# Kernel tuning notes

Hardware: AMD Instinct MI355X
Metric: run time of the kernel (lower is better)

The kernel has to match this reference:

```python
import jax, jax.numpy as jnp
import numpy as np

B, S, D = 2, 4096, 4096          # batch, seq, hidden == qkv_output_dim
R = 16                            # LoRA rank
BOTTLE = 64                       # policy bottleneck
SCALING = 2.0                     # all_scalings for both adapters
CAT = 2 * D                       # input_multiplier = 1 + num_active_adapters(=1)


def setup_inputs() -> dict:
    key = jax.random.key(0)
    ks = jax.random.split(key, 16)
    s = 0.02
    return {
        "x": jax.random.normal(ks[0], (B, S, D), jnp.float32),
        "base_out": jax.random.normal(ks[1], (B, S, D), jnp.float32),
        # LoRA banks: A [r, hidden], B [out, r]
        "A_pos": jax.random.normal(ks[2], (R, D), jnp.float32) * s,
        "B_pos": jax.random.normal(ks[3], (D, R), jnp.float32) * s,
        "A_neg": jax.random.normal(ks[4], (R, D), jnp.float32) * s,
        "B_neg": jax.random.normal(ks[5], (D, R), jnp.float32) * s,
        # policy direction net: Linear(CAT->64) -> ReLU -> Linear(64->D)
        "W1": jax.random.normal(ks[6], (BOTTLE, CAT), jnp.float32) * s,
        "b1": jnp.zeros((BOTTLE,), jnp.float32),
        "W2": jax.random.normal(ks[7], (D, BOTTLE), jnp.float32) * s,
        "b2": jnp.zeros((D,), jnp.float32),
        # policy gate net: Linear(CAT->64) -> ReLU -> Linear(64->1)
        "G1": jax.random.normal(ks[8], (BOTTLE, CAT), jnp.float32) * s,
        "g1": jnp.zeros((BOTTLE,), jnp.float32),
        "G2": jax.random.normal(ks[9], (1, BOTTLE), jnp.float32) * 0.01,
        "g2": jnp.zeros((1,), jnp.float32),
    }


def reference(x, base_out, A_pos, B_pos, A_neg, B_neg,
              W1, b1, W2, b2, G1, g1, G2, g2):
    # hook_fn: sum of two LoRA deltas (low-rank: contract to rank first)
    lora = ((x @ A_pos.T) @ B_pos.T) * SCALING + ((x @ A_neg.T) @ B_neg.T) * SCALING  # [B,S,D]
    # FusionPolicy with a single (summed) adapter input
    cat_input = jnp.concatenate([base_out, lora], axis=-1)  # [B,S,2D]
    residual_base = lora
    h = jax.nn.relu(cat_input @ W1.T + b1)                  # [B,S,64]
    direction = h @ W2.T + b2 + residual_base               # [B,S,D]
    hg = jax.nn.relu(cat_input @ G1.T + g1)                 # [B,S,64]
    alpha = jax.nn.sigmoid((hg @ G2.T + g2) * 6.0)          # [B,S,1]
    fusion_delta = direction * alpha
    return base_out + fusion_delta
```

## Files before the change

kernel.cpp:

```cpp
#include <hip/hip_runtime.h>
#include <math.h>

#define BSROWS 8192
#define DD 4096
#define CATD 8192
#define NB 64
#define NP1 160
#define PS 164
#define HS 104
#define KOUT 96

typedef __attribute__((ext_vector_type(8))) short bf16x8;
typedef __attribute__((ext_vector_type(4))) float f32x4;

static __device__ __forceinline__ unsigned short f2bf(float f) {
  union { float f; unsigned u; } v; v.f = f;
  unsigned r = v.u + 0x7FFFu + ((v.u >> 16) & 1u);
  return (unsigned short)(r >> 16);
}

static __device__ __forceinline__ bf16x8 pack8(const float* __restrict__ p) {
  float4 a = *(const float4*)p;
  float4 b = *(const float4*)(p + 4);
  bf16x8 r;
  r[0] = (short)f2bf(a.x); r[1] = (short)f2bf(a.y);
  r[2] = (short)f2bf(a.z); r[3] = (short)f2bf(a.w);
  r[4] = (short)f2bf(b.x); r[5] = (short)f2bf(b.y);
  r[6] = (short)f2bf(b.z); r[7] = (short)f2bf(b.w);
  return r;
}

__global__ void prep_weights(const float* __restrict__ A_pos, const float* __restrict__ A_neg,
                             const float* __restrict__ W1, const float* __restrict__ G1,
                             const float* __restrict__ W2, const float* __restrict__ B_pos,
                             const float* __restrict__ B_neg,
                             unsigned short* __restrict__ Wp1, unsigned short* __restrict__ Wout) {
  int tid = blockIdx.x * blockDim.x + threadIdx.x;
  const int total = NP1 * DD + DD * KOUT;
  for (int e = tid; e < total; e += gridDim.x * blockDim.x) {
    if (e < NP1 * DD) {
      int n = e >> 12, k = e & 4095;
      float v;
      if (n < 16)      v = A_pos[n * DD + k];
      else if (n < 32) v = A_neg[(n - 16) * DD + k];
      else if (n < 96) v = W1[(n - 32) * CATD + k];
      else             v = G1[(n - 96) * CATD + k];
      Wp1[e] = f2bf(v);
    } else {
      int e2 = e - NP1 * DD;
      int n = e2 / KOUT, j = e2 - n * KOUT;
      float v;
      if (j < NB) v = W2[n * NB + j];
      else {
        int i = j - NB;
        v = 2.f * ((i < 16) ? B_pos[n * 16 + i] : B_neg[n * 16 + (i - 16)]);
      }
      Wout[e2] = f2bf(v);
    }
  }
}

__global__ void prep_m_partial(const float* __restrict__ B_pos, const float* __restrict__ B_neg,
                               const float* __restrict__ W1, const float* __restrict__ G1,
                               float* __restrict__ part) {
  int t = blockIdx.x * 256 + threadIdx.x;
  int chunk = t >> 12;
  int rem = t & 4095;
  int net = rem >> 11;
  int i = (rem >> 6) & 31;
  int j = rem & 63;
  const float* Bp = (i < 16) ? (B_pos + i) : (B_neg + (i - 16));
  const float* Wr = ((net == 0) ? W1 : G1) + (size_t)j * CATD + DD;
  float acc = 0.f;
  int d0 = chunk * 512;
#pragma unroll 8
  for (int d = 0; d < 512; ++d) acc += Bp[(size_t)(d0 + d) * 16] * Wr[d0 + d];
  part[t] = 2.f * acc;
}

__global__ void prep_m_reduce(const float* __restrict__ part,
                              float* __restrict__ M1, float* __restrict__ M2) {
  int t = blockIdx.x * 256 + threadIdx.x;
  int net = t >> 11;
  int ij = t & 2047;
  float s = 0.f;
#pragma unroll
  for (int c = 0; c < 8; ++c) s += part[c * 4096 + net * 2048 + ij];
  (net == 0 ? M1 : M2)[ij] = s;
}

__global__ __launch_bounds__(512, 4)
void fused_main(const float* __restrict__ x, const float* __restrict__ base,
                const unsigned short* __restrict__ Wp1, const unsigned short* __restrict__ Wout,
                const float* __restrict__ M1, const float* __restrict__ M2,
                const float* __restrict__ b1, const float* __restrict__ g1,
                const float* __restrict__ b2f, const float* __restrict__ G2,
                const float* __restrict__ g2, float* __restrict__ out) {
  __shared__ __align__(16) float P[2][16][PS];
  __shared__ __align__(16) unsigned short Hcat[16][HS];
  __shared__ float alpha_s[16];

  const int tid = threadIdx.x;
  const int w = tid >> 6;
  const int lane = tid & 63;
  const int col = lane & 15;
  const int kseg = (lane >> 4) * 8;
  const int kh = w >> 2;
  const int wsub = w & 3;
  const long row0 = (long)blockIdx.x * 16;

  const float* xrow = x + (row0 + col) * DD;
  const float* brow = base + (row0 + col) * DD;

  f32x4 acc0 = {0.f, 0.f, 0.f, 0.f};
  f32x4 acc1 = {0.f, 0.f, 0.f, 0.f};
  f32x4 acc2 = {0.f, 0.f, 0.f, 0.f};
  const bool hasx = (wsub < 2);
  const int kbeg = kh * 2048;
#pragma unroll 2
  for (int k0 = kbeg; k0 < kbeg + 2048; k0 += 32) {
    const int kk = k0 + kseg;
    bf16x8 ba = pack8(brow + kk);
    bf16x8 a0;
    if (hasx) a0 = pack8(xrow + kk); else a0 = ba;
    const unsigned short* wp = Wp1 + kk;
    bf16x8 bw0 = *(const bf16x8*)(wp + (size_t)(wsub * 16 + col) * DD);
    bf16x8 bw1 = *(const bf16x8*)(wp + (size_t)((wsub + 4) * 16 + col) * DD);
    acc0 = __builtin_amdgcn_mfma_f32_16x16x32_bf16(a0, bw0, acc0, 0, 0, 0);
    acc1 = __builtin_amdgcn_mfma_f32_16x16x32_bf16(ba, bw1, acc1, 0, 0, 0);
    if (hasx) {
      bf16x8 bw2 = *(const bf16x8*)(wp + (size_t)((wsub + 8) * 16 + col) * DD);
      acc2 = __builtin_amdgcn_mfma_f32_16x16x32_bf16(ba, bw2, acc2, 0, 0, 0);
    }
  }
  {
    const int rbase = (lane >> 4) * 4;
#pragma unroll
    for (int r = 0; r < 4; ++r) {
      P[kh][rbase + r][wsub * 16 + col] = acc0[r];
      P[kh][rbase + r][(wsub + 4) * 16 + col] = acc1[r];
      if (hasx) P[kh][rbase + r][(wsub + 8) * 16 + col] = acc2[r];
    }
  }
  __syncthreads();

  if (tid < 256) {
    const int row = tid >> 4, jg = tid & 15;
    float tl[32];
#pragma unroll
    for (int i = 0; i < 32; ++i) tl[i] = P[0][row][i] + P[1][row][i];
    float hv[4];
    float partg = 0.f;
#pragma unroll
    for (int jj = 0; jj < 4; ++jj) {
      const int j = jg * 4 + jj;
      float s1 = b1[j] + P[0][row][32 + j] + P[1][row][32 + j];
      float s2 = g1[j] + P[0][row][96 + j] + P[1][row][96 + j];
#pragma unroll
      for (int i = 0; i < 32; ++i) {
        s1 += tl[i] * M1[i * 64 + j];
        s2 += tl[i] * M2[i * 64 + j];
      }
      hv[jj] = fmaxf(s1, 0.f);
      partg += G2[j] * fmaxf(s2, 0.f);
    }
#pragma unroll
    for (int m = 8; m >= 1; m >>= 1) partg += __shfl_xor(partg, m);
    const float alpha = 1.f / (1.f + expf(-6.f * (partg + g2[0])));
    if (jg == 0) alpha_s[row] = alpha;
#pragma unroll
    for (int jj = 0; jj < 4; ++jj) Hcat[row][jg * 4 + jj] = f2bf(alpha * hv[jj]);
    if (jg < 8) {
#pragma unroll
      for (int ii = 0; ii < 4; ++ii)
        Hcat[row][64 + jg * 4 + ii] = f2bf(alpha * tl[jg * 4 + ii]);
    }
  }
  __syncthreads();

  bf16x8 af0 = *(const bf16x8*)&Hcat[col][kseg];
  bf16x8 af1 = *(const bf16x8*)&Hcat[col][32 + kseg];
  bf16x8 af2 = *(const bf16x8*)&Hcat[col][64 + kseg];
  const int rbase = (lane >> 4) * 4;
  float al[4];
#pragma unroll
  for (int r = 0; r < 4; ++r) al[r] = alpha_s[rbase + r];

  for (int i = 0; i < 32; ++i) {
    const int nt = w + 8 * i;
    const int gcol = nt * 16 + col;
    const unsigned short* wo = Wout + (size_t)gcol * KOUT;
    bf16x8 w0 = *(const bf16x8*)(wo + kseg);
    bf16x8 w1v = *(const bf16x8*)(wo + 32 + kseg);
    bf16x8 w2v = *(const bf16x8*)(wo + 64 + kseg);
    f32x4 c = {0.f, 0.f, 0.f, 0.f};
    c = __builtin_amdgcn_mfma_f32_16x16x32_bf16(af0, w0, c, 0, 0, 0);
    c = __builtin_amdgcn_mfma_f32_16x16x32_bf16(af1, w1v, c, 0, 0, 0);
    c = __builtin_amdgcn_mfma_f32_16x16x32_bf16(af2, w2v, c, 0, 0, 0);
    const float bb = b2f[gcol];
#pragma unroll
    for (int r = 0; r < 4; ++r) {
      const size_t off = (size_t)(row0 + rbase + r) * DD + gcol;
      out[off] = base[off] + c[r] + al[r] * bb;
    }
  }
}

extern "C" void kernel_launch(void* const* d_in, const int* in_sizes, int n_in,
                              void* d_out, int out_size, void* d_ws, size_t ws_size,
                              hipStream_t stream) {
  const float* x     = (const float*)d_in[0];
  const float* base  = (const float*)d_in[1];
  const float* A_pos = (const float*)d_in[2];
  const float* B_pos = (const float*)d_in[3];
  const float* A_neg = (const float*)d_in[4];
  const float* B_neg = (const float*)d_in[5];
  const float* W1    = (const float*)d_in[6];
  const float* b1    = (const float*)d_in[7];
  const float* W2    = (const float*)d_in[8];
  const float* b2    = (const float*)d_in[9];
  const float* G1    = (const float*)d_in[10];
  const float* g1    = (const float*)d_in[11];
  const float* G2    = (const float*)d_in[12];
  const float* g2    = (const float*)d_in[13];
  float* out = (float*)d_out;

  char* ws = (char*)d_ws;
  unsigned short* Wp1  = (unsigned short*)(ws);
  unsigned short* Wout = (unsigned short*)(ws + 1310720);
  float* M1   = (float*)(ws + 2097152);
  float* M2   = (float*)(ws + 2105344);
  float* part = (float*)(ws + 2113536);

  prep_weights<<<1024, 256, 0, stream>>>(A_pos, A_neg, W1, G1, W2, B_pos, B_neg, Wp1, Wout);
  prep_m_partial<<<128, 256, 0, stream>>>(B_pos, B_neg, W1, G1, part);
  prep_m_reduce<<<16, 256, 0, stream>>>(part, M1, M2);
  fused_main<<<512, 512, 0, stream>>>(x, base, Wp1, Wout, M1, M2, b1, g1, b2, G2, g2, out);
}
```

Before: 547.9 us.

## Split fused main kernel into panel, policy and output GEMM stages for more parallelism

The single fused kernel, one block per 16-row tile and 512 blocks total, is split into three kernels. panel_P splits K across two blocks and writes partial projections to global memory. policy_rows computes the gate and hidden activations per row. out_gemm splits the output columns four ways across 2048 blocks. The M-matrix precompute also becomes a single warp-reduction kernel instead of partial plus reduce. The aim is more blocks and occupancy on the many-CU GPU, at the cost of extra global round trips for the partial sums and Hcat, extra launches, and base being read twice.

```diff
diff --git a/kernel.cpp b/kernel.cpp
--- a/kernel.cpp
+++ b/kernel.cpp
@@ -7,7 +7,6 @@
 #define NB 64
 #define NP1 160
 #define PS 164
-#define HS 104
 #define KOUT 96
 
 typedef __attribute__((ext_vector_type(8))) short bf16x8;
@@ -60,45 +59,28 @@
   }
 }
 
-__global__ void prep_m_partial(const float* __restrict__ B_pos, const float* __restrict__ B_neg,
-                               const float* __restrict__ W1, const float* __restrict__ G1,
-                               float* __restrict__ part) {
-  int t = blockIdx.x * 256 + threadIdx.x;
-  int chunk = t >> 12;
-  int rem = t & 4095;
-  int net = rem >> 11;
-  int i = (rem >> 6) & 31;
-  int j = rem & 63;
+__global__ __launch_bounds__(256, 8)
+void prep_m(const float* __restrict__ B_pos, const float* __restrict__ B_neg,
+            const float* __restrict__ W1, const float* __restrict__ G1,
+            float* __restrict__ M1, float* __restrict__ M2) {
+  const int wid = blockIdx.x * 4 + (threadIdx.x >> 6);
+  const int lane = threadIdx.x & 63;
+  const int net = wid >> 11, ij = wid & 2047;
+  const int i = ij >> 6, j = ij & 63;
   const float* Bp = (i < 16) ? (B_pos + i) : (B_neg + (i - 16));
   const float* Wr = ((net == 0) ? W1 : G1) + (size_t)j * CATD + DD;
   float acc = 0.f;
-  int d0 = chunk * 512;
-#pragma unroll 8
-  for (int d = 0; d < 512; ++d) acc += Bp[(size_t)(d0 + d) * 16] * Wr[d0 + d];
-  part[t] = 2.f * acc;
-}
-
-__global__ void prep_m_reduce(const float* __restrict__ part,
-                              float* __restrict__ M1, float* __restrict__ M2) {
-  int t = blockIdx.x * 256 + threadIdx.x;
-  int net = t >> 11;
-  int ij = t & 2047;
-  float s = 0.f;
-#pragma unroll
-  for (int c = 0; c < 8; ++c) s += part[c * 4096 + net * 2048 + ij];
-  (net == 0 ? M1 : M2)[ij] = s;
-}
-
-__global__ __launch_bounds__(512, 4)
-void fused_main(const float* __restrict__ x, const float* __restrict__ base,
-                const unsigned short* __restrict__ Wp1, const unsigned short* __restrict__ Wout,
-                const float* __restrict__ M1, const float* __restrict__ M2,
-                const float* __restrict__ b1, const float* __restrict__ g1,
-                const float* __restrict__ b2f, const float* __restrict__ G2,
-                const float* __restrict__ g2, float* __restrict__ out) {
+  for (int d = lane; d < DD; d += 64)
+    acc += Bp[(size_t)d * 16] * Wr[d];
+#pragma unroll
+  for (int m = 32; m >= 1; m >>= 1) acc += __shfl_xor(acc, m);
+  if (lane == 0) (net == 0 ? M1 : M2)[ij] = 2.f * acc;
+}
+
+__global__ __launch_bounds__(512, 8)
+void panel_P(const float* __restrict__ x, const float* __restrict__ base,
+             const unsigned short* __restrict__ Wp1, float* __restrict__ Ppart) {
   __shared__ __align__(16) float P[2][16][PS];
-  __shared__ __align__(16) unsigned short Hcat[16][HS];
-  __shared__ float alpha_s[16];
 
   const int tid = threadIdx.x;
   const int w = tid >> 6;
@@ -107,7 +89,9 @@
   const int kseg = (lane >> 4) * 8;
   const int kh = w >> 2;
   const int wsub = w & 3;
-  const long row0 = (long)blockIdx.x * 16;
+  const int tile = blockIdx.x >> 1;
+  const int bkh = blockIdx.x & 1;
+  const long row0 = (long)tile * 16;
 
   const float* xrow = x + (row0 + col) * DD;
   const float* brow = base + (row0 + col) * DD;
@@ -116,9 +100,9 @@
   f32x4 acc1 = {0.f, 0.f, 0.f, 0.f};
   f32x4 acc2 = {0.f, 0.f, 0.f, 0.f};
   const bool hasx = (wsub < 2);
-  const int kbeg = kh * 2048;
+  const int kbeg = bkh * 2048 + kh * 1024;
 #pragma unroll 2
-  for (int k0 = kbeg; k0 < kbeg + 2048; k0 += 32) {
+  for (int k0 = kbeg; k0 < kbeg + 1024; k0 += 32) {
     const int kk = k0 + kseg;
     bf16x8 ba = pack8(brow + kk);
     bf16x8 a0;
@@ -146,48 +130,94 @@
 
   if (tid < 256) {
     const int row = tid >> 4, jg = tid & 15;
-    float tl[32];
-#pragma unroll
-    for (int i = 0; i < 32; ++i) tl[i] = P[0][row][i] + P[1][row][i];
-    float hv[4];
-    float partg = 0.f;
-#pragma unroll
-    for (int jj = 0; jj < 4; ++jj) {
-      const int j = jg * 4 + jj;
-      float s1 = b1[j] + P[0][row][32 + j] + P[1][row][32 + j];
-      float s2 = g1[j] + P[0][row][96 + j] + P[1][row][96 + j];
-#pragma unroll
-      for (int i = 0; i < 32; ++i) {
-        s1 += tl[i] * M1[i * 64 + j];
-        s2 += tl[i] * M2[i * 64 + j];
-      }
-      hv[jj] = fmaxf(s1, 0.f);
-      partg += G2[j] * fmaxf(s2, 0.f);
-    }
-#pragma unroll
-    for (int m = 8; m >= 1; m >>= 1) partg += __shfl_xor(partg, m);
-    const float alpha = 1.f / (1.f + expf(-6.f * (partg + g2[0])));
-    if (jg == 0) alpha_s[row] = alpha;
-#pragma unroll
-    for (int jj = 0; jj < 4; ++jj) Hcat[row][jg * 4 + jj] = f2bf(alpha * hv[jj]);
-    if (jg < 8) {
-#pragma unroll
-      for (int ii = 0; ii < 4; ++ii)
-        Hcat[row][64 + jg * 4 + ii] = f2bf(alpha * tl[jg * 4 + ii]);
-    }
-  }
+    float* dst = Ppart + (((size_t)bkh * 512 + tile) * 16 + row) * 160;
+#pragma unroll
+    for (int q = 0; q < 10; ++q) {
+      const int c = q * 16 + jg;
+      dst[c] = P[0][row][c] + P[1][row][c];
+    }
+  }
+}
+
+__global__ __launch_bounds__(256, 8)
+void policy_rows(const float* __restrict__ Ppart, const float* __restrict__ M1,
+                 const float* __restrict__ M2, const float* __restrict__ b1,
+                 const float* __restrict__ g1, const float* __restrict__ G2,
+                 const float* __restrict__ g2,
+                 unsigned short* __restrict__ Hcat, float* __restrict__ alphaG) {
+  const int gtid = blockIdx.x * 256 + threadIdx.x;
+  const int rowg = gtid >> 4;
+  const int jg = gtid & 15;
+  const float* P0 = Ppart + (size_t)rowg * 160;
+  const float* P1 = Ppart + (size_t)(8192 + rowg) * 160;
+
+  float tv[32];
+#pragma unroll
+  for (int i = 0; i < 32; ++i) tv[i] = P0[i] + P1[i];
+  float hv[4];
+  float partg = 0.f;
+#pragma unroll
+  for (int jj = 0; jj < 4; ++jj) {
+    const int j = jg * 4 + jj;
+    float s1 = b1[j] + P0[32 + j] + P1[32 + j];
+    float s2 = g1[j] + P0[96 + j] + P1[96 + j];
+#pragma unroll
+    for (int i = 0; i < 32; ++i) {
+      s1 += tv[i] * M1[i * 64 + j];
+      s2 += tv[i] * M2[i * 64 + j];
+    }
+    hv[jj] = fmaxf(s1, 0.f);
+    partg += G2[j] * fmaxf(s2, 0.f);
+  }
+#pragma unroll
+  for (int m = 8; m >= 1; m >>= 1) partg += __shfl_xor(partg, m);
+  const float alpha = 1.f / (1.f + expf(-6.f * (partg + g2[0])));
+  if (jg == 0) alphaG[rowg] = alpha;
+  unsigned short* hrow = Hcat + (size_t)rowg * 96;
+#pragma unroll
+  for (int jj = 0; jj < 4; ++jj) hrow[jg * 4 + jj] = f2bf(alpha * hv[jj]);
+  if (jg < 8) {
+#pragma unroll
+    for (int ii = 0; ii < 4; ++ii)
+      hrow[64 + jg * 4 + ii] = f2bf(alpha * tv[jg * 4 + ii]);
+  }
+}
+
+__global__ __launch_bounds__(256, 8)
+void out_gemm(const float* __restrict__ base, const unsigned short* __restrict__ Hcat,
+              const float* __restrict__ alphaG, const unsigned short* __restrict__ Wout,
+              const float* __restrict__ b2f, float* __restrict__ out) {
+  __shared__ __align__(16) unsigned short H[16][96];
+  __shared__ float ash[16];
+
+  const int tid = threadIdx.x;
+  const int rt = blockIdx.x >> 2;
+  const int cb = blockIdx.x & 3;
+  const long row0 = (long)rt * 16;
+
+  if (tid < 192) {
+    const int row = tid / 12, seg = tid % 12;
+    *(bf16x8*)&H[row][seg * 8] =
+        *(const bf16x8*)(Hcat + ((size_t)(row0 + row)) * 96 + seg * 8);
+  }
+  if (tid < 16) ash[tid] = alphaG[row0 + tid];
   __syncthreads();
 
-  bf16x8 af0 = *(const bf16x8*)&Hcat[col][kseg];
-  bf16x8 af1 = *(const bf16x8*)&Hcat[col][32 + kseg];
-  bf16x8 af2 = *(const bf16x8*)&Hcat[col][64 + kseg];
+  const int w = tid >> 6;
+  const int lane = tid & 63;
+  const int col = lane & 15;
+  const int kseg = (lane >> 4) * 8;
   const int rbase = (lane >> 4) * 4;
+
+  bf16x8 af0 = *(const bf16x8*)&H[col][kseg];
+  bf16x8 af1 = *(const bf16x8*)&H[col][32 + kseg];
+  bf16x8 af2 = *(const bf16x8*)&H[col][64 + kseg];
   float al[4];
 #pragma unroll
-  for (int r = 0; r < 4; ++r) al[r] = alpha_s[rbase + r];
-
-  for (int i = 0; i < 32; ++i) {
-    const int nt = w + 8 * i;
+  for (int r = 0; r < 4; ++r) al[r] = ash[rbase + r];
+
+  for (int i = 0; i < 16; ++i) {
+    const int nt = cb * 64 + w + 4 * i;
     const int gcol = nt * 16 + col;
     const unsigned short* wo = Wout + (size_t)gcol * KOUT;
     bf16x8 w0 = *(const bf16x8*)(wo + kseg);
@@ -226,14 +256,17 @@
   float* out = (float*)d_out;
 
   char* ws = (char*)d_ws;
-  unsigned short* Wp1  = (unsigned short*)(ws);
-  unsigned short* Wout = (unsigned short*)(ws + 1310720);
-  float* M1   = (float*)(ws + 2097152);
-  float* M2   = (float*)(ws + 2105344);
-  float* part = (float*)(ws + 2113536);
+  unsigned short* Wp1   = (unsigned short*)(ws);
+  unsigned short* Wout  = (unsigned short*)(ws + 1310720);
+  float* M1     = (float*)(ws + 2097152);
+  float* M2     = (float*)(ws + 2105344);
+  float* Ppart  = (float*)(ws + 2113536);
+  unsigned short* Hcat = (unsigned short*)(ws + 12599296);
+  float* alphaG = (float*)(ws + 14172160);
 
   prep_weights<<<1024, 256, 0, stream>>>(A_pos, A_neg, W1, G1, W2, B_pos, B_neg, Wp1, Wout);
-  prep_m_partial<<<128, 256, 0, stream>>>(B_pos, B_neg, W1, G1, part);
-  prep_m_reduce<<<16, 256, 0, stream>>>(part, M1, M2);
-  fused_main<<<512, 512, 0, stream>>>(x, base, Wp1, Wout, M1, M2, b1, g1, b2, G2, g2, out);
-}
+  prep_m<<<1024, 256, 0, stream>>>(B_pos, B_neg, W1, G1, M1, M2);
+  panel_P<<<1024, 512, 0, stream>>>(x, base, Wp1, Ppart);
+  policy_rows<<<512, 256, 0, stream>>>(Ppart, M1, M2, b1, g1, G2, g2, Hcat, alphaG);
+  out_gemm<<<2048, 256, 0, stream>>>(base, Hcat, alphaG, Wout, b2, out);
+}
```

Result: slower. 614.3 us (+12.1%).
